# Kernel optimization log

Measured on AMD Instinct MI355X. Metric: run time of the kernel, lower is better.

The kernel has to match this reference:

```python
import jax, jax.numpy as jnp
import numpy as np

DIM = 1536
NH = 12
HD = 128
EPS = 1e-6


def _rope(x, freqs, f, h, w, start):
    # x: [B,S,N,D] with S == f*h*w; freqs: [1024, D//2, 2] (real, imag) unit rotations
    B, S, N, D = x.shape
    c = D // 2
    c0 = c - 2 * (c // 3)
    c1 = c // 3
    ff = jnp.broadcast_to(freqs[start:start + f, :c0][:, None, None], (f, h, w, c0, 2))
    fh = jnp.broadcast_to(freqs[:h, c0:c0 + c1][None, :, None], (f, h, w, c1, 2))
    fw = jnp.broadcast_to(freqs[:w, c0 + c1:c][None, None, :], (f, h, w, c1, 2))
    fr = jnp.concatenate([ff, fh, fw], axis=3).reshape(S, 1, c, 2)  # [S,1,c,2]
    xr, xi = x[..., 0::2], x[..., 1::2]          # interleaved real/imag pairs
    cr, ci = fr[None, ..., 0], fr[None, ..., 1]  # [1,S,1,c]
    yr = xr * cr - xi * ci
    yi = xr * ci + xi * cr
    return jnp.stack([yr, yi], axis=-1).reshape(B, S, N, D)


def _rms(x, g):
    return x * jax.lax.rsqrt(jnp.mean(x * x, axis=-1, keepdims=True) + EPS) * g


def setup_inputs():
    key = jax.random.key(0)
    ks = jax.random.split(key, 16)
    S = 3 * 30 * 52  # chunk_size = 3 frames * 1560 tokens/frame
    x = jax.random.normal(ks[0], (1, S, DIM), jnp.float32)
    fr = jax.random.normal(ks[1], (1024, HD // 2, 2), jnp.float32)
    fr = fr / jnp.sqrt(jnp.sum(fr * fr, axis=-1, keepdims=True) + 1e-12)  # unit-modulus rotations
    g_kmean = jax.random.uniform(ks[2], (1, NH, HD), jnp.float32)  # mean of relu(k): nonnegative
    g_kv = jax.random.normal(ks[3], (1, NH, HD, HD), jnp.float32) * 0.05
    p = lambda i, shp: jax.random.normal(ks[i], shp, jnp.float32) * 0.02
    return dict(
        x=x, freqs=fr, g_kmean=g_kmean, g_kv=g_kv,
        Wq=p(4, (DIM, DIM)), bq=p(5, (DIM,)),
        Wk=p(6, (DIM, DIM)), bk=p(7, (DIM,)),
        Wv=p(8, (DIM, DIM)), bv=p(9, (DIM,)),
        Wo=p(10, (DIM, DIM)), bo=p(11, (DIM,)),
        gq=jnp.ones((DIM,), jnp.float32), gk=jnp.ones((DIM,), jnp.float32),
        Wlin=p(12, (HD, HD)), blin=p(13, (HD,)),
        f_frames=3, h_grid=30, w_grid=52,
    )


def reference(x, freqs, g_kmean, g_kv, Wq, bq, Wk, bk, Wv, bv, Wo, bo, gq, gk, Wlin, blin, f_frames, h_grid, w_grid):
    B, S, _ = x.shape
    q = _rms(x @ Wq.T + bq, gq).reshape(B, S, NH, HD)
    k = _rms(x @ Wk.T + bk, gk).reshape(B, S, NH, HD)
    v = (x @ Wv.T + bv).reshape(B, S, NH, HD)
    rq = _rope(q, freqs, f_frames, h_grid, w_grid, 0)
    rk = _rope(k, freqs, f_frames, h_grid, w_grid, 0)
    # local window attention: at step 0 (current_start=0, empty cache, sink_size=0)
    # the working kv window is exactly the roped current chunk
    scores = jnp.einsum('bsnd,btnd->bnst', rq, rk) * (HD ** -0.5)
    x_local = jnp.einsum('bnst,btnd->bsnd', jax.nn.softmax(scores, axis=-1), v)
    # global linear-attention branch (kernel_func = relu feature map on q, roped q against kv state)
    qf = jax.nn.relu(q)
    z = 1.0 / (jnp.einsum('bsnd,bnd->bsn', qf, g_kmean) + 1e-6)
    xg = jnp.einsum('bsnd,bndm->bsnm', rq, g_kv) * z[..., None]
    xg = xg @ Wlin.T + blin
    out = (x_local + xg).reshape(B, S, DIM) @ Wo.T + bo
    return out
```

## Files before the change

### kernel.cpp

```cpp
#include <hip/hip_runtime.h>

typedef short s16x8 __attribute__((ext_vector_type(8)));
typedef float f32x4 __attribute__((ext_vector_type(4)));
typedef float f32x16 __attribute__((ext_vector_type(16)));
typedef unsigned short u16x4 __attribute__((ext_vector_type(4)));
typedef unsigned int u32x4 __attribute__((ext_vector_type(4)));

#define QSCALE (0.08838834764831845f * 1.4426950408889634f)

__device__ __forceinline__ unsigned short f2bf(float f) {
  unsigned int u = __float_as_uint(f);
  u += 0x7fffu + ((u >> 16) & 1u);
  return (unsigned short)(u >> 16);
}
__device__ __forceinline__ float bf2f(unsigned short h) {
  return __uint_as_float((unsigned int)h << 16);
}
__device__ __forceinline__ float fast_exp2(float x) {
  float r;
  asm("v_exp_f32 %0, %1" : "=v"(r) : "v"(x));
  return r;
}

__device__ __forceinline__ void gload16(const void* gp, void* lp) {
  __builtin_amdgcn_global_load_lds(
      (const __attribute__((address_space(1))) void*)gp,
      (__attribute__((address_space(3))) void*)lp,
      16, 0, 0);
}

__global__ void cast_f32_bf16_x4(const float* __restrict__ in,
                                 unsigned short* __restrict__ out, int n4) {
  int i = blockIdx.x * 256 + threadIdx.x;
  if (i >= n4) return;
  f32x4 v = *((const f32x4*)in + i);
  u16x4 o;
  o[0] = f2bf(v[0]); o[1] = f2bf(v[1]); o[2] = f2bf(v[2]); o[3] = f2bf(v[3]);
  *((u16x4*)out + i) = o;
}

__global__ void g2fill_kernel(const float* __restrict__ g_kv,
                              const float* __restrict__ Wlin,
                              unsigned short* __restrict__ G2c) {
  int h = blockIdx.x, m = blockIdx.y, d = threadIdx.x;
  const float* gk = g_kv + ((size_t)h * 128 + d) * 128;
  const float* wl = Wlin + (size_t)m * 128;
  float s = 0.f;
  for (int j = 0; j < 128; ++j) s += gk[j] * wl[j];
  G2c[((size_t)h * 128 + m) * 128 + d] = f2bf(s * (1.0f / QSCALE));
}

template <int MODE>
__global__ __launch_bounds__(256) void gemm_bt(
    const unsigned short* __restrict__ A, const unsigned short* __restrict__ B,
    const float* __restrict__ bias, void* __restrict__ Cout,
    int M, int N, int K, int lda, int ldb,
    const float* __restrict__ o0buf, const float* __restrict__ zbuf,
    const float* __restrict__ o1buf, const float* __restrict__ lbuf, int nsplit) {
  __shared__ __align__(16) unsigned short Asm_[128 * 64];
  __shared__ __align__(16) unsigned short Bsm_[128 * 64];
  const int tid = threadIdx.x;
  const int wid = tid >> 6, lane = tid & 63;
  const int mt = blockIdx.x, nt = blockIdx.y;
  const int wr = wid >> 1, wc = wid & 1;
  const int acol = (MODE == 3) ? nt * 128 : 0;
  f32x4 acc[4][4] = {};

  const int st_srccol = ((((lane & 7) << 4) ^ ((lane >> 3) << 4)) >> 1);
  const int st_rowoff = (lane >> 3);

  for (int k0 = 0; k0 < K; k0 += 64) {
    __syncthreads();
#pragma unroll
    for (int r = 0; r < 4; ++r) {
      int c = wid * 4 + r;
      int lrow = c * 8 + st_rowoff;
      int arow = mt * 128 + lrow; if (arow > M - 1) arow = M - 1;
      gload16(A + (size_t)arow * lda + acol + k0 + st_srccol,
              (char*)Asm_ + c * 1024 + lane * 16);
      int brow = nt * 128 + lrow;
      gload16(B + (size_t)brow * ldb + k0 + st_srccol,
              (char*)Bsm_ + c * 1024 + lane * 16);
    }
    __syncthreads();
#pragma unroll
    for (int kk = 0; kk < 2; ++kk) {
      int cb = (kk * 64 + ((lane >> 4) << 4)) ^ ((lane & 7) << 4);
      s16x8 af[4], bfr[4];
#pragma unroll
      for (int m = 0; m < 4; ++m)
        af[m] = *(const s16x8*)((const char*)Asm_ + (wr * 64 + m * 16 + (lane & 15)) * 128 + cb);
#pragma unroll
      for (int n = 0; n < 4; ++n)
        bfr[n] = *(const s16x8*)((const char*)Bsm_ + (wc * 64 + n * 16 + (lane & 15)) * 128 + cb);
#pragma unroll
      for (int m = 0; m < 4; ++m)
#pragma unroll
        for (int n = 0; n < 4; ++n)
          acc[m][n] = __builtin_amdgcn_mfma_f32_16x16x32_bf16(af[m], bfr[n], acc[m][n], 0, 0, 0);
    }
  }
  const int rb = mt * 128 + wr * 64, cbse = nt * 128 + wc * 64;
#pragma unroll
  for (int m = 0; m < 4; ++m) {
#pragma unroll
    for (int n = 0; n < 4; ++n) {
#pragma unroll
      for (int rg = 0; rg < 4; ++rg) {
        int rr = rb + m * 16 + ((lane >> 4) << 2) + rg;
        int cc = cbse + n * 16 + (lane & 15);
        if (rr < M) {
          float v = acc[m][n][rg];
          if (MODE == 0) {
            v += bias[cc];
            ((unsigned short*)Cout)[(size_t)rr * N + cc] = f2bf(v);
          } else if (MODE == 1) {
            v += bias[cc];
            ((float*)Cout)[(size_t)rr * N + cc] = v;
          } else {
            int hd = cc >> 7;
            float lsum = lbuf[(size_t)rr * 12 + hd];
            float osum = o0buf[(size_t)rr * N + cc];
            for (int s = 1; s < nsplit; ++s) {
              lsum += lbuf[((size_t)s * M + rr) * 12 + hd];
              osum += o1buf[(size_t)(s - 1) * M * 1536 + (size_t)rr * N + cc];
            }
            v = v * zbuf[(size_t)rr * 12 + hd] + osum * (1.0f / lsum) + bias[cc & 127];
            ((unsigned short*)Cout)[(size_t)rr * N + cc] = f2bf(v);
          }
        }
      }
    }
  }
}

__global__ __launch_bounds__(256) void rms_rope_kernel(
    const unsigned short* __restrict__ pre, const float* __restrict__ freqs,
    const float* __restrict__ g, const float* __restrict__ g_kmean,
    unsigned short* __restrict__ outr, float* __restrict__ zout,
    int S, int ld, float oscale,
    const int* __restrict__ hgp, const int* __restrict__ wgp) {
  const int s = blockIdx.x;
  const int tid = threadIdx.x;
  const int lane = tid & 63, wid = tid >> 6;
  const unsigned short* row = pre + (size_t)s * ld;
  unsigned int pv0, pv1, pv2;
  float ssq = 0.f;
  {
    pv0 = *(const unsigned int*)(row + 2 * (tid));
    pv1 = *(const unsigned int*)(row + 2 * (tid + 256));
    pv2 = *(const unsigned int*)(row + 2 * (tid + 512));
    float a0 = bf2f((unsigned short)(pv0 & 0xffffu)), b0 = bf2f((unsigned short)(pv0 >> 16));
    float a1 = bf2f((unsigned short)(pv1 & 0xffffu)), b1 = bf2f((unsigned short)(pv1 >> 16));
    float a2 = bf2f((unsigned short)(pv2 & 0xffffu)), b2 = bf2f((unsigned short)(pv2 >> 16));
    ssq = a0 * a0 + b0 * b0 + a1 * a1 + b1 * b1 + a2 * a2 + b2 * b2;
  }
#pragma unroll
  for (int m = 1; m < 64; m <<= 1) ssq += __shfl_xor(ssq, m, 64);
  __shared__ float wpart[4];
  if (lane == 0) wpart[wid] = ssq;
  __syncthreads();
  float tot = wpart[0] + wpart[1] + wpart[2] + wpart[3];
  float rms = rsqrtf(tot * (1.0f / 1536.0f) + 1e-6f);
  const int Wg = *wgp;
  const int HWg = (*hgp) * Wg;
  int fi = s / HWg; int rem = s - fi * HWg;
  int hi = rem / Wg; int wi = rem - hi * Wg;
  unsigned int pvs[3] = {pv0, pv1, pv2};
#pragma unroll
  for (int rd = 0; rd < 3; ++rd) {
    int p = tid + rd * 256;
    int c = p & 63;
    int fidx = (c < 22) ? fi : ((c < 43) ? hi : wi);
    float cr = freqs[fidx * 128 + 2 * c];
    float ci = freqs[fidx * 128 + 2 * c + 1];
    float xr = bf2f((unsigned short)(pvs[rd] & 0xffffu)) * rms * g[2 * p];
    float xi = bf2f((unsigned short)(pvs[rd] >> 16)) * rms * g[2 * p + 1];
    float yr = (xr * cr - xi * ci) * oscale;
    float yi = (xr * ci + xi * cr) * oscale;
    unsigned int ow = (unsigned int)f2bf(yr) | ((unsigned int)f2bf(yi) << 16);
    *(unsigned int*)(outr + (size_t)s * 1536 + 2 * p) = ow;
    if (zout != nullptr) {
      int head = p >> 6;
      float part = fmaxf(xr, 0.f) * g_kmean[head * 128 + 2 * c] +
                   fmaxf(xi, 0.f) * g_kmean[head * 128 + 2 * c + 1];
#pragma unroll
      for (int m = 1; m < 64; m <<= 1) part += __shfl_xor(part, m, 64);
      if (lane == 0) zout[(size_t)s * 12 + head] = 1.0f / (part + 1e-6f);
    }
  }
}

__global__ __launch_bounds__(256) void vtrans_kernel(const unsigned short* __restrict__ vpre,
                                                     unsigned short* __restrict__ vt, int S, int ld) {
  __shared__ unsigned short tile[64][66];
  int t0 = blockIdx.x * 64, c0 = blockIdx.y * 64;
  int tid = threadIdx.x;
#pragma unroll
  for (int rep = 0; rep < 16; ++rep) {
    int lin = rep * 256 + tid;
    int i = lin >> 6, j = lin & 63;
    int t = t0 + i; if (t > S - 1) t = S - 1;
    tile[i][j] = vpre[(size_t)t * ld + c0 + j];
  }
  __syncthreads();
#pragma unroll
  for (int rep = 0; rep < 16; ++rep) {
    int lin = rep * 256 + tid;
    int j = lin >> 6, i = lin & 63;
    int t = t0 + i;
    if (t < S) vt[(size_t)(c0 + j) * S + t] = tile[i][j];
  }
}

__global__ __launch_bounds__(256, 3) void attn_kernel(
    const unsigned short* __restrict__ rq, const unsigned short* __restrict__ rk,
    const unsigned short* __restrict__ vt, float* __restrict__ o0buf,
    float* __restrict__ o1buf, float* __restrict__ lbuf, int S, int nqb, int nsplit) {
  __shared__ __align__(16) unsigned short Ks[2][32 * 128];
  __shared__ __align__(16) unsigned short Vs[2][128 * 32];
  const int tid = threadIdx.x, wid = tid >> 6, lane = tid & 63;
  const int q32 = lane & 31, hi = lane >> 5;

  const int total = nqb * 12 * nsplit;
  int lg = blockIdx.x;
  if ((total & 7) == 0) lg = (lg & 7) * (total >> 3) + (lg >> 3);
  const int z = lg / (nqb * 12);
  int rem = lg - z * nqb * 12;
  const int h = rem / nqb;
  const int qb = rem - h * nqb;
  const int q0 = qb * 128 + wid * 32;

  const int seg = (((S + nsplit - 1) / nsplit) + 31) & ~31;
  const int tbeg = z * seg;
  const int tend = (tbeg + seg < S) ? (tbeg + seg) : S;
  float* obufz = (z == 0) ? o0buf : (o1buf + (size_t)(z - 1) * S * 1536);
  float* lbufz = lbuf + (size_t)z * S * 12;

  s16x8 qf[8];
  {
    int qrow = q0 + q32; if (qrow > S - 1) qrow = S - 1;
    const unsigned short* qp = rq + (size_t)qrow * 1536 + h * 128 + hi * 8;
#pragma unroll
    for (int dblk = 0; dblk < 8; ++dblk) qf[dblk] = *(const s16x8*)(qp + dblk * 16);
  }
  f32x16 o0 = {}, o1 = {}, o2 = {}, o3 = {};
  float lsum = 0.f;

  const int k_tok0 = tid >> 4;
  const int k_off = (tid & 15) * 16;
  const int v_d0 = tid >> 2;
  const int v_toff = (tid & 3) * 16;
  const int vswz = ((q32 >> 1) & 3) << 4;

#define STAGE(buf, t0s)                                                            \
  {                                                                                \
    _Pragma("unroll") for (int r = 0; r < 2; ++r) {                                \
      int ktok = k_tok0 + 16 * r;                                                  \
      int kb = k_off ^ ((ktok & 7) << 4);                                          \
      int trow = (t0s) + ktok; if (trow > S - 1) trow = S - 1;                     \
      gload16(rk + (size_t)trow * 1536 + h * 128 + (kb >> 1),                      \
              (char*)Ks[buf] + r * 4096 + tid * 16);                               \
      int dd = v_d0 + 64 * r;                                                      \
      int vb_ = v_toff ^ (((dd >> 1) & 3) << 4);                                   \
      int vtok = (t0s) + (vb_ >> 1); if (vtok > S - 8) vtok = S - 8;               \
      gload16(vt + (size_t)(h * 128 + dd) * S + vtok,                              \
              (char*)Vs[buf] + r * 4096 + tid * 16);                               \
    }                                                                              \
  }

  STAGE(0, tbeg);
  __syncthreads();
  int cur = 0;
  for (int t0 = tbeg; t0 < tend; t0 += 32) {
    if (t0 + 32 < tend) STAGE(cur ^ 1, t0 + 32);
    f32x16 sc = {};
    __builtin_amdgcn_s_setprio(1);
#pragma unroll
    for (int dblk = 0; dblk < 8; ++dblk) {
      s16x8 kfr = *(const s16x8*)((const char*)Ks[cur] + q32 * 256 +
                                  ((dblk * 32 + hi * 16) ^ ((q32 & 7) << 4)));
      sc = __builtin_amdgcn_mfma_f32_32x32x16_bf16(kfr, qf[dblk], sc, 0, 0, 0);
    }
    __builtin_amdgcn_s_setprio(0);
    const bool full = (t0 + 32 <= tend);
    unsigned int pk[8];
    float rs = 0.f;
#pragma unroll
    for (int j = 0; j < 8; ++j) {
      float p0, p1;
      if (full) {
        p0 = fast_exp2(sc[2 * j]);
        p1 = fast_exp2(sc[2 * j + 1]);
      } else {
        int r0 = 2 * j;
        int tk0 = t0 + (r0 & 3) + 8 * (r0 >> 2) + 4 * hi;
        p0 = (tk0 < tend) ? fast_exp2(sc[2 * j]) : 0.f;
        p1 = (tk0 + 1 < tend) ? fast_exp2(sc[2 * j + 1]) : 0.f;
      }
      unsigned int u0 = __float_as_uint(p0) & 0xffff0000u;
      unsigned int u1 = __float_as_uint(p1) & 0xffff0000u;
      rs += __uint_as_float(u0) + __uint_as_float(u1);
      pk[j] = (u0 >> 16) | u1;
    }
    lsum += rs;
    unsigned int x0 = pk[0], y0 = pk[2], x1 = pk[1], y1 = pk[3];
    asm("v_permlane32_swap_b32 %0, %1" : "+v"(x0), "+v"(y0));
    asm("v_permlane32_swap_b32 %0, %1" : "+v"(x1), "+v"(y1));
    unsigned int x2 = pk[4], y2 = pk[6], x3 = pk[5], y3 = pk[7];
    asm("v_permlane32_swap_b32 %0, %1" : "+v"(x2), "+v"(y2));
    asm("v_permlane32_swap_b32 %0, %1" : "+v"(x3), "+v"(y3));
    u32x4 pa0v = {x0, x1, y0, y1};
    u32x4 pa1v = {x2, x3, y2, y3};
    s16x8 pa0 = __builtin_bit_cast(s16x8, pa0v);
    s16x8 pa1 = __builtin_bit_cast(s16x8, pa1v);
    __builtin_amdgcn_s_setprio(1);
#pragma unroll
    for (int ks = 0; ks < 2; ++ks) {
      s16x8 pa = ks ? pa1 : pa0;
      const int tb = (ks * 32 + hi * 16) ^ vswz;
      const char* vbase = (const char*)Vs[cur] + q32 * 64 + tb;
      s16x8 vb;
      vb = *(const s16x8*)(vbase + 0 * 2048);
      o0 = __builtin_amdgcn_mfma_f32_32x32x16_bf16(pa, vb, o0, 0, 0, 0);
      vb = *(const s16x8*)(vbase + 1 * 2048);
      o1 = __builtin_amdgcn_mfma_f32_32x32x16_bf16(pa, vb, o1, 0, 0, 0);
      vb = *(const s16x8*)(vbase + 2 * 2048);
      o2 = __builtin_amdgcn_mfma_f32_32x32x16_bf16(pa, vb, o2, 0, 0, 0);
      vb = *(const s16x8*)(vbase + 3 * 2048);
      o3 = __builtin_amdgcn_mfma_f32_32x32x16_bf16(pa, vb, o3, 0, 0, 0);
    }
    __builtin_amdgcn_s_setprio(0);
    __syncthreads();
    cur ^= 1;
  }
  lsum += __shfl_xor(lsum, 32, 64);
  {
    int qrow = q0 + q32;
    if (hi == 0 && qrow < S) lbufz[(size_t)qrow * 12 + h] = lsum;
  }
#pragma unroll
  for (int r = 0; r < 16; ++r) {
    int qrow = q0 + (r & 3) + 8 * (r >> 2) + 4 * hi;
    if (qrow < S) {
      float* orow = obufz + (size_t)qrow * 1536 + h * 128 + q32;
      orow[0] = o0[r]; orow[32] = o1[r]; orow[64] = o2[r]; orow[96] = o3[r];
    }
  }
#undef STAGE
}

extern "C" void kernel_launch(void* const* d_in, const int* in_sizes, int n_in,
                              void* d_out, int out_size, void* d_ws, size_t ws_size,
                              hipStream_t stream) {
  const float* x = (const float*)d_in[0];
  const float* freqs = (const float*)d_in[1];
  const float* g_kmean = (const float*)d_in[2];
  const float* g_kv = (const float*)d_in[3];
  const float* Wq = (const float*)d_in[4];  const float* bq = (const float*)d_in[5];
  const float* Wk = (const float*)d_in[6];  const float* bk = (const float*)d_in[7];
  const float* Wv = (const float*)d_in[8];  const float* bv = (const float*)d_in[9];
  const float* Wo = (const float*)d_in[10]; const float* bo = (const float*)d_in[11];
  const float* gq = (const float*)d_in[12]; const float* gk = (const float*)d_in[13];
  const float* Wlin = (const float*)d_in[14]; const float* blin = (const float*)d_in[15];
  const int* hgp = (const int*)d_in[17];
  const int* wgp = (const int*)d_in[18];

  const int S = in_sizes[0] / 1536;

  char* ws = (char*)d_ws;
  const size_t SZ = (size_t)S * 1536 * 2;
  const size_t OSZ = (size_t)S * 1536 * 4;
  const size_t WSZ = (size_t)1536 * 1536 * 2;
  const size_t QKVSZ = (size_t)S * 4608 * 2;
  const size_t G2SZ = (size_t)12 * 128 * 128 * 2;
  size_t o_xbf = 0;
  size_t o_wqkv = o_xbf + SZ;
  size_t o_wo = o_wqkv + 3 * WSZ;
  size_t o_g2 = o_wo + WSZ;
  size_t o_qkv = o_g2 + G2SZ;
  size_t o_rk = o_qkv + QKVSZ;
  size_t o_vt = o_rk + SZ;
  size_t o_z = o_vt + SZ;
  size_t o_bqkv = o_z + (size_t)S * 12 * 4;
  size_t o_o1 = o_bqkv + 4608 * 4;

  int nsplit = 4;
  if (ws_size < o_o1 + (size_t)3 * OSZ + (size_t)4 * S * 12 * 4) nsplit = 2;
  size_t o_l = o_o1 + (size_t)(nsplit - 1) * OSZ;
  size_t need = o_l + (size_t)nsplit * S * 12 * 4;
  if (ws_size < need) return;

  unsigned short* xbf = (unsigned short*)(ws + o_xbf);
  unsigned short* wqkv = (unsigned short*)(ws + o_wqkv);
  unsigned short* wob = (unsigned short*)(ws + o_wo);
  unsigned short* g2c = (unsigned short*)(ws + o_g2);
  unsigned short* qkv = (unsigned short*)(ws + o_qkv);
  unsigned short* rkb = (unsigned short*)(ws + o_rk);
  unsigned short* vtb = (unsigned short*)(ws + o_vt);
  float* zbuf = (float*)(ws + o_z);
  float* bqkv = (float*)(ws + o_bqkv);
  unsigned short* rqb = xbf;
  float* o0buf = (float*)(ws + o_qkv);
  float* o1buf = (float*)(ws + o_o1);
  float* lbuf = (float*)(ws + o_l);
  unsigned short* ybf = (unsigned short*)(ws + o_qkv + OSZ);

  {
    int n4 = (S * 1536) / 4;
    cast_f32_bf16_x4<<<(n4 + 255) / 256, 256, 0, stream>>>(x, xbf, n4);
    int w4 = (1536 * 1536) / 4;
    int wg = (w4 + 255) / 256;
    cast_f32_bf16_x4<<<wg, 256, 0, stream>>>(Wq, wqkv, w4);
    cast_f32_bf16_x4<<<wg, 256, 0, stream>>>(Wk, wqkv + (size_t)1536 * 1536, w4);
    cast_f32_bf16_x4<<<wg, 256, 0, stream>>>(Wv, wqkv + (size_t)2 * 1536 * 1536, w4);
    cast_f32_bf16_x4<<<wg, 256, 0, stream>>>(Wo, wob, w4);
  }
  hipMemcpyAsync(bqkv, bq, 1536 * 4, hipMemcpyDeviceToDevice, stream);
  hipMemcpyAsync(bqkv + 1536, bk, 1536 * 4, hipMemcpyDeviceToDevice, stream);
  hipMemcpyAsync(bqkv + 3072, bv, 1536 * 4, hipMemcpyDeviceToDevice, stream);

  g2fill_kernel<<<dim3(12, 128), 128, 0, stream>>>(g_kv, Wlin, g2c);

  {
    dim3 ggrid((S + 127) / 128, 36);
    gemm_bt<0><<<ggrid, 256, 0, stream>>>(xbf, wqkv, bqkv, qkv, S, 4608, 1536, 1536, 1536,
                                          nullptr, nullptr, nullptr, nullptr, 0);
  }

  rms_rope_kernel<<<S, 256, 0, stream>>>(qkv, freqs, gq, g_kmean, rqb, zbuf, S, 4608, QSCALE, hgp, wgp);
  rms_rope_kernel<<<S, 256, 0, stream>>>(qkv + 1536, freqs, gk, nullptr, rkb, nullptr, S, 4608, 1.0f, hgp, wgp);

  vtrans_kernel<<<dim3((S + 63) / 64, 24), 256, 0, stream>>>(qkv + 3072, vtb, S, 4608);

  {
    int nqb = (S + 127) / 128;
    attn_kernel<<<dim3(nqb * 12 * nsplit), 256, 0, stream>>>(rqb, rkb, vtb,
                                                             o0buf, o1buf, lbuf, S, nqb, nsplit);
  }

  {
    dim3 ggrid((S + 127) / 128, 12);
    gemm_bt<3><<<ggrid, 256, 0, stream>>>(rqb, g2c, blin, ybf, S, 1536, 128, 1536, 128,
                                          o0buf, zbuf, o1buf, lbuf, nsplit);
    gemm_bt<1><<<ggrid, 256, 0, stream>>>(ybf, wob, bo, (float*)d_out, S, 1536, 1536, 1536, 1536,
                                          nullptr, nullptr, nullptr, nullptr, 0);
  }
}
```

Measured before the change: 464.5 us.

## Merge weight casts and q/k rms-rope launches, template split count

After: 408.4 us. 12.1% less time.

```diff
diff --git a/kernel.cpp b/kernel.cpp
--- a/kernel.cpp
+++ b/kernel.cpp
@@ -37,6 +37,20 @@
   u16x4 o;
   o[0] = f2bf(v[0]); o[1] = f2bf(v[1]); o[2] = f2bf(v[2]); o[3] = f2bf(v[3]);
   *((u16x4*)out + i) = o;
+}
+
+__global__ void cast_weights4(const float* __restrict__ Wq, const float* __restrict__ Wk,
+                              const float* __restrict__ Wv, const float* __restrict__ Wo,
+                              unsigned short* __restrict__ dst, int per4) {
+  int i = blockIdx.x * 256 + threadIdx.x;
+  if (i >= 4 * per4) return;
+  int m = i / per4;
+  int off = i - m * per4;
+  const float* src = (m == 0) ? Wq : (m == 1) ? Wk : (m == 2) ? Wv : Wo;
+  f32x4 v = *((const f32x4*)src + off);
+  u16x4 o;
+  o[0] = f2bf(v[0]); o[1] = f2bf(v[1]); o[2] = f2bf(v[2]); o[3] = f2bf(v[3]);
+  *((u16x4*)dst + i) = o;
 }
 
 __global__ void g2fill_kernel(const float* __restrict__ g_kv,
@@ -50,13 +64,13 @@
   G2c[((size_t)h * 128 + m) * 128 + d] = f2bf(s * (1.0f / QSCALE));
 }
 
-template <int MODE>
+template <int MODE, int NSPLIT>
 __global__ __launch_bounds__(256) void gemm_bt(
     const unsigned short* __restrict__ A, const unsigned short* __restrict__ B,
     const float* __restrict__ bias, void* __restrict__ Cout,
     int M, int N, int K, int lda, int ldb,
     const float* __restrict__ o0buf, const float* __restrict__ zbuf,
-    const float* __restrict__ o1buf, const float* __restrict__ lbuf, int nsplit) {
+    const float* __restrict__ o1buf, const float* __restrict__ lbuf) {
   __shared__ __align__(16) unsigned short Asm_[128 * 64];
   __shared__ __align__(16) unsigned short Bsm_[128 * 64];
   const int tid = threadIdx.x;
@@ -121,7 +135,8 @@
             int hd = cc >> 7;
             float lsum = lbuf[(size_t)rr * 12 + hd];
             float osum = o0buf[(size_t)rr * N + cc];
-            for (int s = 1; s < nsplit; ++s) {
+#pragma unroll
+            for (int s = 1; s < NSPLIT; ++s) {
               lsum += lbuf[((size_t)s * M + rr) * 12 + hd];
               osum += o1buf[(size_t)(s - 1) * M * 1536 + (size_t)rr * N + cc];
             }
@@ -135,15 +150,21 @@
 }
 
 __global__ __launch_bounds__(256) void rms_rope_kernel(
-    const unsigned short* __restrict__ pre, const float* __restrict__ freqs,
-    const float* __restrict__ g, const float* __restrict__ g_kmean,
-    unsigned short* __restrict__ outr, float* __restrict__ zout,
-    int S, int ld, float oscale,
+    const unsigned short* __restrict__ qkv, const float* __restrict__ freqs,
+    const float* __restrict__ gq, const float* __restrict__ gk,
+    const float* __restrict__ g_kmean,
+    unsigned short* __restrict__ rqb, unsigned short* __restrict__ rkb,
+    float* __restrict__ zbuf, int S,
     const int* __restrict__ hgp, const int* __restrict__ wgp) {
   const int s = blockIdx.x;
+  const int isk = blockIdx.y;
+  const unsigned short* row = qkv + (size_t)s * 4608 + (isk ? 1536 : 0);
+  const float* g = isk ? gk : gq;
+  unsigned short* outr = isk ? rkb : rqb;
+  float* zout = isk ? nullptr : zbuf;
+  const float oscale = isk ? 1.0f : QSCALE;
   const int tid = threadIdx.x;
   const int lane = tid & 63, wid = tid >> 6;
-  const unsigned short* row = pre + (size_t)s * ld;
   unsigned int pv0, pv1, pv2;
   float ssq = 0.f;
   {
@@ -385,8 +406,8 @@
   size_t o_bqkv = o_z + (size_t)S * 12 * 4;
   size_t o_o1 = o_bqkv + 4608 * 4;
 
-  int nsplit = 4;
-  if (ws_size < o_o1 + (size_t)3 * OSZ + (size_t)4 * S * 12 * 4) nsplit = 2;
+  int nsplit = 3;
+  if (ws_size < o_o1 + (size_t)2 * OSZ + (size_t)3 * S * 12 * 4) nsplit = 2;
   size_t o_l = o_o1 + (size_t)(nsplit - 1) * OSZ;
   size_t need = o_l + (size_t)nsplit * S * 12 * 4;
   if (ws_size < need) return;
@@ -409,12 +430,8 @@
   {
     int n4 = (S * 1536) / 4;
     cast_f32_bf16_x4<<<(n4 + 255) / 256, 256, 0, stream>>>(x, xbf, n4);
-    int w4 = (1536 * 1536) / 4;
-    int wg = (w4 + 255) / 256;
-    cast_f32_bf16_x4<<<wg, 256, 0, stream>>>(Wq, wqkv, w4);
-    cast_f32_bf16_x4<<<wg, 256, 0, stream>>>(Wk, wqkv + (size_t)1536 * 1536, w4);
-    cast_f32_bf16_x4<<<wg, 256, 0, stream>>>(Wv, wqkv + (size_t)2 * 1536 * 1536, w4);
-    cast_f32_bf16_x4<<<wg, 256, 0, stream>>>(Wo, wob, w4);
+    int per4 = (1536 * 1536) / 4;
+    cast_weights4<<<(4 * per4 + 255) / 256, 256, 0, stream>>>(Wq, Wk, Wv, Wo, wqkv, per4);
   }
   hipMemcpyAsync(bqkv, bq, 1536 * 4, hipMemcpyDeviceToDevice, stream);
   hipMemcpyAsync(bqkv + 1536, bk, 1536 * 4, hipMemcpyDeviceToDevice, stream);
@@ -424,12 +441,12 @@
 
   {
     dim3 ggrid((S + 127) / 128, 36);
-    gemm_bt<0><<<ggrid, 256, 0, stream>>>(xbf, wqkv, bqkv, qkv, S, 4608, 1536, 1536, 1536,
-                                          nullptr, nullptr, nullptr, nullptr, 0);
-  }
-
-  rms_rope_kernel<<<S, 256, 0, stream>>>(qkv, freqs, gq, g_kmean, rqb, zbuf, S, 4608, QSCALE, hgp, wgp);
-  rms_rope_kernel<<<S, 256, 0, stream>>>(qkv + 1536, freqs, gk, nullptr, rkb, nullptr, S, 4608, 1.0f, hgp, wgp);
+    gemm_bt<0, 2><<<ggrid, 256, 0, stream>>>(xbf, wqkv, bqkv, qkv, S, 4608, 1536, 1536, 1536,
+                                             nullptr, nullptr, nullptr, nullptr);
+  }
+
+  rms_rope_kernel<<<dim3(S, 2), 256, 0, stream>>>(qkv, freqs, gq, gk, g_kmean,
+                                                  rqb, rkb, zbuf, S, hgp, wgp);
 
   vtrans_kernel<<<dim3((S + 63) / 64, 24), 256, 0, stream>>>(qkv + 3072, vtb, S, 4608);
 
@@ -441,9 +458,14 @@
 
   {
     dim3 ggrid((S + 127) / 128, 12);
-    gemm_bt<3><<<ggrid, 256, 0, stream>>>(rqb, g2c, blin, ybf, S, 1536, 128, 1536, 128,
-                                          o0buf, zbuf, o1buf, lbuf, nsplit);
-    gemm_bt<1><<<ggrid, 256, 0, stream>>>(ybf, wob, bo, (float*)d_out, S, 1536, 1536, 1536, 1536,
-                                          nullptr, nullptr, nullptr, nullptr, 0);
-  }
-}
+    if (nsplit == 3) {
+      gemm_bt<3, 3><<<ggrid, 256, 0, stream>>>(rqb, g2c, blin, ybf, S, 1536, 128, 1536, 128,
+                                               o0buf, zbuf, o1buf, lbuf);
+    } else {
+      gemm_bt<3, 2><<<ggrid, 256, 0, stream>>>(rqb, g2c, blin, ybf, S, 1536, 128, 1536, 128,
+                                               o0buf, zbuf, o1buf, lbuf);
+    }
+    gemm_bt<1, 2><<<ggrid, 256, 0, stream>>>(ybf, wob, bo, (float*)d_out, S, 1536, 1536, 1536, 1536,
+                                             nullptr, nullptr, nullptr, nullptr);
+  }
+}
```
